# Optimization experiments

Measured on AMD Instinct MI355X. Metric: run time of the kernel, lower is better.

The kernel has to match this reference:

```python
import jax, jax.numpy as jnp
import numpy as np

D_MODEL = 1024
NUM_HEADS = 16
DEPTH = D_MODEL // NUM_HEADS
B, S = 2, 2048


def setup_inputs() -> dict:
    key = jax.random.key(0)
    ks = jax.random.split(key, 13)
    scale = 1.0 / np.sqrt(D_MODEL)
    inp = {
        "v": jax.random.normal(ks[0], (B, S, D_MODEL), jnp.float32),
        "k": jax.random.normal(ks[1], (B, S, D_MODEL), jnp.float32),
        "q": jax.random.normal(ks[2], (B, S, D_MODEL), jnp.float32),
        # additive 0/1 mask, broadcast over heads
        "mask": jax.random.randint(ks[3], (B, 1, S, S), 0, 2).astype(jnp.float32),
        "wq": jax.random.normal(ks[4], (D_MODEL, D_MODEL), jnp.float32) * scale,
        "bq": jnp.zeros((D_MODEL,), jnp.float32),
        "wk": jax.random.normal(ks[5], (D_MODEL, D_MODEL), jnp.float32) * scale,
        "bk": jnp.zeros((D_MODEL,), jnp.float32),
        "wv": jax.random.normal(ks[6], (D_MODEL, D_MODEL), jnp.float32) * scale,
        "bv": jnp.zeros((D_MODEL,), jnp.float32),
        "wo": jax.random.normal(ks[7], (D_MODEL, D_MODEL), jnp.float32) * scale,
        "bo": jnp.zeros((D_MODEL,), jnp.float32),
    }
    return inp


def _split_heads(x):
    # [B, S, D] -> [B, H, S, depth]
    b, s, _ = x.shape
    return x.reshape(b, s, NUM_HEADS, DEPTH).transpose(0, 2, 1, 3)


def reference(v, k, q, mask, wq, bq, wk, bk, wv, bv, wo, bo):
    # torch Linear: y = x @ W.T + b
    qh = _split_heads(q @ wq.T + bq)
    kh = _split_heads(k @ wk.T + bk)
    vh = _split_heads(v @ wv.T + bv)
    score = jnp.einsum("bhqd,bhkd->bhqk", qh, kh) / jnp.sqrt(jnp.float32(DEPTH))
    score = score + mask * jnp.float32(-1e9)
    attn = jax.nn.softmax(score, axis=-1)
    out = jnp.einsum("bhqk,bhkd->bhqd", attn, vh)
    out = out.transpose(0, 2, 1, 3).reshape(out.shape[0], -1, D_MODEL)
    return out @ wo.T + bo
```

## Files before the change

kernel.cpp:

```cpp
#include <hip/hip_runtime.h>


typedef float f32x4 __attribute__((ext_vector_type(4)));
typedef __bf16 bf16x8 __attribute__((ext_vector_type(8)));
typedef unsigned short u16x8 __attribute__((ext_vector_type(8)));

#define DEV static __device__ __forceinline__

DEV unsigned short f2bf(float x) {
  return __builtin_bit_cast(unsigned short, static_cast<__bf16>(x));
}
DEV bf16x8 ld8(const unsigned short* p) {
  return __builtin_bit_cast(bf16x8, *reinterpret_cast<const u16x8*>(p));
}
DEV f32x4 mfma16(bf16x8 a, bf16x8 b, f32x4 c) {
  return __builtin_amdgcn_mfma_f32_16x16x32_bf16(a, b, c, 0, 0, 0);
}
DEV void gl2lds16(const unsigned short* g, unsigned short* l) {
  __builtin_amdgcn_global_load_lds(
      (const __attribute__((address_space(1))) void*)g,
      (__attribute__((address_space(3))) void*)l, 16, 0, 0);
}

__global__ __launch_bounds__(256)
void cvt3(const float* __restrict__ a, const float* __restrict__ b,
          const float* __restrict__ c, unsigned short* __restrict__ oa,
          unsigned short* __restrict__ ob, unsigned short* __restrict__ oc)
{
  const float* in;
  unsigned short* out;
  if (blockIdx.y == 0) { in = a; out = oa; }
  else if (blockIdx.y == 1) { in = b; out = ob; }
  else { in = c; out = oc; }
  const size_t i = (size_t)blockIdx.x * 256 + threadIdx.x;
  const f32x4* p = (const f32x4*)(in + i * 8);
  f32x4 x = p[0], y = p[1];
  u16x8 u;
#pragma unroll
  for (int j = 0; j < 4; ++j) u[j] = f2bf(x[j]);
#pragma unroll
  for (int j = 0; j < 4; ++j) u[4 + j] = f2bf(y[j]);
  *(u16x8*)(out + i * 8) = u;
}

__global__ __launch_bounds__(256)
void cvt4(const float* __restrict__ a, const float* __restrict__ b,
          const float* __restrict__ c, const float* __restrict__ d,
          unsigned short* __restrict__ oa, unsigned short* __restrict__ ob,
          unsigned short* __restrict__ oc, unsigned short* __restrict__ od)
{
  const float* in;
  unsigned short* out;
  if (blockIdx.y == 0) { in = a; out = oa; }
  else if (blockIdx.y == 1) { in = b; out = ob; }
  else if (blockIdx.y == 2) { in = c; out = oc; }
  else { in = d; out = od; }
  const size_t i = (size_t)blockIdx.x * 256 + threadIdx.x;
  const f32x4* p = (const f32x4*)(in + i * 8);
  f32x4 x = p[0], y = p[1];
  u16x8 u;
#pragma unroll
  for (int j = 0; j < 4; ++j) u[j] = f2bf(x[j]);
#pragma unroll
  for (int j = 0; j < 4; ++j) u[4 + j] = f2bf(y[j]);
  *(u16x8*)(out + i * 8) = u;
}

__global__ __launch_bounds__(256)
void mask_bits(const float* __restrict__ m, unsigned long long* __restrict__ bits)
{
  const int l = threadIdx.x & 63;
  int w = blockIdx.x * 4 + (threadIdx.x >> 6);
#pragma unroll 1
  for (int i = 0; i < 16; ++i, w += 8192) {
    float v = m[(size_t)w * 64 + l];
    unsigned long long bl = __ballot(v != 0.0f);
    if (l == 0) bits[w] = bl;
  }
}

template<int MODE>
__global__ __launch_bounds__(256)
void gemm_bf16(const unsigned short* __restrict__ Ab,
               const unsigned short* __restrict__ Wb,
               const float* __restrict__ bias, void* __restrict__ outg,
               float scale)
{
  __shared__ unsigned short lA[128 * 64];
  __shared__ unsigned short lB[64 * 64];
  const int tid = threadIdx.x, lane = tid & 63, wid = tid >> 6;
  const int lr = lane & 15, lg = lane >> 4;
  const int wr = wid >> 1, wc = wid & 1;
  const int mbase = blockIdx.y * 128, nbase = blockIdx.x * 64;
  const int rsub = lane >> 3;
  const int colsw = ((lane & 7) ^ rsub) * 8;

  const f32x4 zf = {0.f, 0.f, 0.f, 0.f};
  f32x4 acc[4][2];
#pragma unroll
  for (int i = 0; i < 4; ++i)
#pragma unroll
    for (int j = 0; j < 2; ++j) acc[i][j] = zf;

  for (int kt = 0; kt < 16; ++kt) {
    const int k0 = kt * 64;
#pragma unroll
    for (int i = 0; i < 4; ++i) {
      const int c = wid + 4 * i;
      const int row = c * 8 + rsub;
      gl2lds16(Ab + (size_t)(mbase + row) * 1024 + k0 + colsw, &lA[c * 512]);
    }
#pragma unroll
    for (int i = 0; i < 2; ++i) {
      const int c = wid + 4 * i;
      const int row = c * 8 + rsub;
      gl2lds16(Wb + (size_t)(nbase + row) * 1024 + k0 + colsw, &lB[c * 512]);
    }
    __syncthreads();

#pragma unroll
    for (int kk = 0; kk < 2; ++kk) {
      const int sw = (((kk * 4 + lg) ^ (lr & 7)) * 8);
      bf16x8 a[4], bb[2];
#pragma unroll
      for (int mi = 0; mi < 4; ++mi)
        a[mi] = ld8(&lA[(wr * 64 + mi * 16 + lr) * 64 + sw]);
#pragma unroll
      for (int ni = 0; ni < 2; ++ni)
        bb[ni] = ld8(&lB[(wc * 32 + ni * 16 + lr) * 64 + sw]);
#pragma unroll
      for (int mi = 0; mi < 4; ++mi)
#pragma unroll
        for (int ni = 0; ni < 2; ++ni)
          acc[mi][ni] = mfma16(a[mi], bb[ni], acc[mi][ni]);
    }
    __syncthreads();
  }

#pragma unroll
  for (int ni = 0; ni < 2; ++ni) {
    const int n = nbase + wc * 32 + ni * 16 + lr;
    const float bv = bias[n];
#pragma unroll
    for (int mi = 0; mi < 4; ++mi) {
#pragma unroll
      for (int r = 0; r < 4; ++r) {
        const int m = mbase + wr * 64 + mi * 16 + lg * 4 + r;
        const float val = (acc[mi][ni][r] + bv) * scale;
        if (MODE == 0) {
          const int b = m >> 11, s = m & 2047, h = n >> 6, d = n & 63;
          ((unsigned short*)outg)[(((size_t)((b * 16 + h) * 2048 + s)) << 6) + d] = f2bf(val);
        } else if (MODE == 1) {
          const int b = m >> 11, s = m & 2047, h = n >> 6, d = n & 63;
          ((unsigned short*)outg)[(((size_t)((b * 16 + h) * 64 + d)) << 11) + s] = f2bf(val);
        } else {
          ((float*)outg)[(size_t)m * 1024 + n] = val;
        }
      }
    }
  }
}

__global__ __launch_bounds__(256)
void attn_fwd(const unsigned short* __restrict__ Qh,
              const unsigned short* __restrict__ Kh,
              const unsigned short* __restrict__ Vt,
              const unsigned long long* __restrict__ bits,
              unsigned short* __restrict__ Ao)
{
  __shared__ unsigned short lK[64][72];
  __shared__ unsigned short lV[64][72];
  __shared__ unsigned short lP[4][16][72];
  const int tid = threadIdx.x, lane = tid & 63, wid = tid >> 6;
  const int lr = lane & 15, lg = lane >> 4;
  const int bh = blockIdx.y;
  const int b = bh >> 4, h = bh & 15;
  const size_t head = (size_t)bh << 17;
  const int qw = blockIdx.x * 64 + wid * 16;

  bf16x8 aq[2];
  {
    const u16x8* qp = (const u16x8*)(Qh + head + ((size_t)(qw + lr) << 6));
    aq[0] = __builtin_bit_cast(bf16x8, qp[lg]);
    aq[1] = __builtin_bit_cast(bf16x8, qp[4 + lg]);
  }

  const f32x4 zf = {0.f, 0.f, 0.f, 0.f};
  f32x4 o[4];
#pragma unroll
  for (int i = 0; i < 4; ++i) o[i] = zf;
  float m_run[4], l_run[4];
#pragma unroll
  for (int r = 0; r < 4; ++r) { m_run[r] = -3.0e38f; l_run[r] = 0.f; }

  const unsigned long long* bptr = bits + ((size_t)b * 2048 + qw) * 32;

  for (int t = 0; t < 32; ++t) {
    const int kv0 = t * 64;
#pragma unroll
    for (int i = 0; i < 2; ++i) {
      int c = tid + 256 * i;
      int row = c >> 3, c8 = c & 7;
      *reinterpret_cast<u16x8*>(&lK[row][c8 * 8]) =
          *(const u16x8*)(Kh + head + ((size_t)(kv0 + row) << 6) + c8 * 8);
      *reinterpret_cast<u16x8*>(&lV[row][c8 * 8]) =
          *(const u16x8*)(Vt + head + ((size_t)row << 11) + kv0 + c8 * 8);
    }
    __syncthreads();

    f32x4 sf[4];
#pragma unroll
    for (int f = 0; f < 4; ++f) {
      f32x4 z = zf;
      z = mfma16(aq[0], ld8(&lK[f * 16 + lr][lg * 8]), z);
      z = mfma16(aq[1], ld8(&lK[f * 16 + lr][32 + lg * 8]), z);
      sf[f] = z;
    }

    float p[4][4];
#pragma unroll
    for (int r = 0; r < 4; ++r) {
      const unsigned long long mb = bptr[(size_t)(lg * 4 + r) * 32 + t];
      float s0 = sf[0][r] - (((mb >> (lr)) & 1) ? 1e9f : 0.f);
      float s1 = sf[1][r] - (((mb >> (16 + lr)) & 1) ? 1e9f : 0.f);
      float s2 = sf[2][r] - (((mb >> (32 + lr)) & 1) ? 1e9f : 0.f);
      float s3 = sf[3][r] - (((mb >> (48 + lr)) & 1) ? 1e9f : 0.f);
      float mx = fmaxf(fmaxf(s0, s1), fmaxf(s2, s3));
      mx = fmaxf(mx, __shfl_xor(mx, 1));
      mx = fmaxf(mx, __shfl_xor(mx, 2));
      mx = fmaxf(mx, __shfl_xor(mx, 4));
      mx = fmaxf(mx, __shfl_xor(mx, 8));
      const float mn = fmaxf(m_run[r], mx);
      const float fac = __expf(m_run[r] - mn);
      m_run[r] = mn;
      float p0 = __expf(s0 - mn), p1 = __expf(s1 - mn);
      float p2 = __expf(s2 - mn), p3 = __expf(s3 - mn);
      p[0][r] = p0; p[1][r] = p1; p[2][r] = p2; p[3][r] = p3;
      float lt = p0 + p1 + p2 + p3;
      lt += __shfl_xor(lt, 1);
      lt += __shfl_xor(lt, 2);
      lt += __shfl_xor(lt, 4);
      lt += __shfl_xor(lt, 8);
      l_run[r] = l_run[r] * fac + lt;
#pragma unroll
      for (int fd = 0; fd < 4; ++fd) o[fd][r] *= fac;
    }

#pragma unroll
    for (int f = 0; f < 4; ++f)
#pragma unroll
      for (int r = 0; r < 4; ++r)
        lP[wid][lg * 4 + r][f * 16 + lr] = f2bf(p[f][r]);

    bf16x8 pa0 = ld8(&lP[wid][lr][lg * 8]);
    bf16x8 pa1 = ld8(&lP[wid][lr][32 + lg * 8]);
#pragma unroll
    for (int fd = 0; fd < 4; ++fd) {
      o[fd] = mfma16(pa0, ld8(&lV[fd * 16 + lr][lg * 8]), o[fd]);
      o[fd] = mfma16(pa1, ld8(&lV[fd * 16 + lr][32 + lg * 8]), o[fd]);
    }
    __syncthreads();
  }

  float inv[4];
#pragma unroll
  for (int r = 0; r < 4; ++r) inv[r] = 1.0f / l_run[r];
  unsigned short* op = Ao + (((size_t)(b * 2048 + blockIdx.x * 64 + wid * 16)) << 10) + h * 64;
#pragma unroll
  for (int fd = 0; fd < 4; ++fd)
#pragma unroll
    for (int r = 0; r < 4; ++r)
      op[((size_t)(lg * 4 + r) << 10) + fd * 16 + lr] = f2bf(o[fd][r] * inv[r]);
}

extern "C" void kernel_launch(void* const* d_in, const int* in_sizes, int n_in,
                              void* d_out, int out_size, void* d_ws, size_t ws_size,
                              hipStream_t stream) {
  const float* v    = (const float*)d_in[0];
  const float* k    = (const float*)d_in[1];
  const float* q    = (const float*)d_in[2];
  const float* mask = (const float*)d_in[3];
  const float* wq = (const float*)d_in[4];  const float* bq = (const float*)d_in[5];
  const float* wk = (const float*)d_in[6];  const float* bk = (const float*)d_in[7];
  const float* wv = (const float*)d_in[8];  const float* bv = (const float*)d_in[9];
  const float* wo = (const float*)d_in[10]; const float* bo = (const float*)d_in[11];

  unsigned short* ws = (unsigned short*)d_ws;
  const size_t T = 4194304;
  unsigned short* Qh  = ws;
  unsigned short* Kh  = ws + T;
  unsigned short* Vt  = ws + 2 * T;
  unsigned short* Ao  = ws + 3 * T;
  unsigned short* Qb  = ws + 4 * T;
  unsigned short* Kb  = ws + 5 * T;
  unsigned short* Vb  = ws + 6 * T;
  unsigned short* Wqb = ws + 7 * T;
  unsigned short* Wkb = Wqb + 1048576;
  unsigned short* Wvb = Wkb + 1048576;
  unsigned short* Wob = Wvb + 1048576;
  unsigned long long* bits = (unsigned long long*)(ws + 8 * T);

  dim3 blk(256);
  cvt3<<<dim3(2048, 3), blk, 0, stream>>>(q, k, v, Qb, Kb, Vb);
  cvt4<<<dim3(512, 4), blk, 0, stream>>>(wq, wk, wv, wo, Wqb, Wkb, Wvb, Wob);
  mask_bits<<<dim3(2048), blk, 0, stream>>>(mask, bits);

  dim3 gg(16, 32);
  gemm_bf16<0><<<gg, blk, 0, stream>>>(Qb, Wqb, bq, Qh, 0.125f);
  gemm_bf16<0><<<gg, blk, 0, stream>>>(Kb, Wkb, bk, Kh, 1.0f);
  gemm_bf16<1><<<gg, blk, 0, stream>>>(Vb, Wvb, bv, Vt, 1.0f);

  attn_fwd<<<dim3(32, 32), blk, 0, stream>>>(Qh, Kh, Vt, bits, Ao);

  gemm_bf16<2><<<gg, blk, 0, stream>>>(Ao, Wob, bo, d_out, 1.0f);
}
```

Before: 341.4 us.

## Transpose attention score layout, swizzle LDS with direct global-to-LDS loads, batch Q/K GEMMs

The attention kernel now computes S^T by swapping the MFMA operands, so each lane holds one query row. Softmax max and sum need only two cross-lane shuffles per tile instead of four per row, and the mask is read once per lane. K and V tiles are loaded straight into XOR-swizzled LDS with global_load_lds instead of going through registers into padded arrays, and P is written with vector stores into a swizzled buffer. The Q and K projection GEMMs are merged into one launch via blockIdx.z, which adds some per-block pointer selection and relies on the swizzle index maths being correct.

```diff
diff --git a/kernel.cpp b/kernel.cpp
--- a/kernel.cpp
+++ b/kernel.cpp
@@ -4,6 +4,7 @@
 typedef float f32x4 __attribute__((ext_vector_type(4)));
 typedef __bf16 bf16x8 __attribute__((ext_vector_type(8)));
 typedef unsigned short u16x8 __attribute__((ext_vector_type(8)));
+typedef unsigned short u16x4 __attribute__((ext_vector_type(4)));
 
 #define DEV static __device__ __forceinline__
 
@@ -81,11 +82,19 @@
 
 template<int MODE>
 __global__ __launch_bounds__(256)
-void gemm_bf16(const unsigned short* __restrict__ Ab,
-               const unsigned short* __restrict__ Wb,
-               const float* __restrict__ bias, void* __restrict__ outg,
-               float scale)
-{
+void gemm_bf16(const unsigned short* __restrict__ A0,
+               const unsigned short* __restrict__ W0,
+               const float* __restrict__ b0, void* __restrict__ o0, float sc0,
+               const unsigned short* __restrict__ A1,
+               const unsigned short* __restrict__ W1,
+               const float* __restrict__ b1, void* __restrict__ o1, float sc1)
+{
+  const unsigned short* Ab = blockIdx.z ? A1 : A0;
+  const unsigned short* Wb = blockIdx.z ? W1 : W0;
+  const float* bias = blockIdx.z ? b1 : b0;
+  void* outg = blockIdx.z ? o1 : o0;
+  const float scale = blockIdx.z ? sc1 : sc0;
+
   __shared__ unsigned short lA[128 * 64];
   __shared__ unsigned short lB[64 * 64];
   const int tid = threadIdx.x, lane = tid & 63, wid = tid >> 6;
@@ -168,11 +177,14 @@
               const unsigned long long* __restrict__ bits,
               unsigned short* __restrict__ Ao)
 {
-  __shared__ unsigned short lK[64][72];
-  __shared__ unsigned short lV[64][72];
-  __shared__ unsigned short lP[4][16][72];
+  __shared__ unsigned short lK[64 * 64];
+  __shared__ unsigned short lV[64 * 64];
+  __shared__ unsigned short lP[4 * 1024];
   const int tid = threadIdx.x, lane = tid & 63, wid = tid >> 6;
   const int lr = lane & 15, lg = lane >> 4;
+  const int a7 = lr & 7;
+  const int rsub = lane >> 3;
+  const int colsw = ((lane & 7) ^ rsub) * 8;
   const int bh = blockIdx.y;
   const int b = bh >> 4, h = bh & 15;
   const size_t head = (size_t)bh << 17;
@@ -189,88 +201,101 @@
   f32x4 o[4];
 #pragma unroll
   for (int i = 0; i < 4; ++i) o[i] = zf;
-  float m_run[4], l_run[4];
-#pragma unroll
-  for (int r = 0; r < 4; ++r) { m_run[r] = -3.0e38f; l_run[r] = 0.f; }
+  float m_run = -3.0e38f, l_run = 0.f;
 
   const unsigned long long* bptr = bits + ((size_t)b * 2048 + qw) * 32;
+  const int g0 = (lg ^ a7) * 8;
+  const int g1 = ((4 + lg) ^ a7) * 8;
 
   for (int t = 0; t < 32; ++t) {
     const int kv0 = t * 64;
 #pragma unroll
     for (int i = 0; i < 2; ++i) {
-      int c = tid + 256 * i;
-      int row = c >> 3, c8 = c & 7;
-      *reinterpret_cast<u16x8*>(&lK[row][c8 * 8]) =
-          *(const u16x8*)(Kh + head + ((size_t)(kv0 + row) << 6) + c8 * 8);
-      *reinterpret_cast<u16x8*>(&lV[row][c8 * 8]) =
-          *(const u16x8*)(Vt + head + ((size_t)row << 11) + kv0 + c8 * 8);
+      const int c = wid + 4 * i;
+      gl2lds16(Kh + head + (size_t)(kv0 + c * 8 + rsub) * 64 + colsw, &lK[c * 512]);
+      gl2lds16(Vt + head + (size_t)(c * 8 + rsub) * 2048 + kv0 + colsw, &lV[c * 512]);
     }
     __syncthreads();
 
     f32x4 sf[4];
 #pragma unroll
     for (int f = 0; f < 4; ++f) {
-      f32x4 z = zf;
-      z = mfma16(aq[0], ld8(&lK[f * 16 + lr][lg * 8]), z);
-      z = mfma16(aq[1], ld8(&lK[f * 16 + lr][32 + lg * 8]), z);
-      sf[f] = z;
-    }
-
-    float p[4][4];
+      const int row = (f * 16 + lr) * 64;
+      f32x4 z = mfma16(ld8(&lK[row + g0]), aq[0], zf);
+      sf[f] = mfma16(ld8(&lK[row + g1]), aq[1], z);
+    }
+
+    const unsigned long long mq = bptr[lr * 32 + t] >> (lg * 4);
+#pragma unroll
+    for (int f = 0; f < 4; ++f) {
+      const unsigned nib = (unsigned)(mq >> (f * 16)) & 0xFu;
+#pragma unroll
+      for (int r = 0; r < 4; ++r)
+        sf[f][r] -= ((nib >> r) & 1u) ? 1e9f : 0.0f;
+    }
+
+    f32x4 mm;
+#pragma unroll
+    for (int r = 0; r < 4; ++r)
+      mm[r] = fmaxf(fmaxf(sf[0][r], sf[1][r]), fmaxf(sf[2][r], sf[3][r]));
+    float mx = fmaxf(fmaxf(mm[0], mm[1]), fmaxf(mm[2], mm[3]));
+    mx = fmaxf(mx, __shfl_xor(mx, 16));
+    mx = fmaxf(mx, __shfl_xor(mx, 32));
+
+    const float mn = fmaxf(m_run, mx);
+    const float fac = __expf(m_run - mn);
+    m_run = mn;
+
+    f32x4 psum = zf;
+    u16x4 pw[4];
+#pragma unroll
+    for (int f = 0; f < 4; ++f) {
+#pragma unroll
+      for (int r = 0; r < 4; ++r) {
+        const float pv = __expf(sf[f][r] - mn);
+        psum[r] += pv;
+        pw[f][r] = f2bf(pv);
+      }
+    }
+    float lt = (psum[0] + psum[1]) + (psum[2] + psum[3]);
+    lt += __shfl_xor(lt, 16);
+    lt += __shfl_xor(lt, 32);
+    l_run = l_run * fac + lt;
+
+#pragma unroll
+    for (int f = 0; f < 4; ++f) {
+      const int g = ((f * 2 + (lg >> 1)) ^ a7) * 8 + (lg & 1) * 4;
+      *(u16x4*)&lP[wid * 1024 + lr * 64 + g] = pw[f];
+    }
+
 #pragma unroll
     for (int r = 0; r < 4; ++r) {
-      const unsigned long long mb = bptr[(size_t)(lg * 4 + r) * 32 + t];
-      float s0 = sf[0][r] - (((mb >> (lr)) & 1) ? 1e9f : 0.f);
-      float s1 = sf[1][r] - (((mb >> (16 + lr)) & 1) ? 1e9f : 0.f);
-      float s2 = sf[2][r] - (((mb >> (32 + lr)) & 1) ? 1e9f : 0.f);
-      float s3 = sf[3][r] - (((mb >> (48 + lr)) & 1) ? 1e9f : 0.f);
-      float mx = fmaxf(fmaxf(s0, s1), fmaxf(s2, s3));
-      mx = fmaxf(mx, __shfl_xor(mx, 1));
-      mx = fmaxf(mx, __shfl_xor(mx, 2));
-      mx = fmaxf(mx, __shfl_xor(mx, 4));
-      mx = fmaxf(mx, __shfl_xor(mx, 8));
-      const float mn = fmaxf(m_run[r], mx);
-      const float fac = __expf(m_run[r] - mn);
-      m_run[r] = mn;
-      float p0 = __expf(s0 - mn), p1 = __expf(s1 - mn);
-      float p2 = __expf(s2 - mn), p3 = __expf(s3 - mn);
-      p[0][r] = p0; p[1][r] = p1; p[2][r] = p2; p[3][r] = p3;
-      float lt = p0 + p1 + p2 + p3;
-      lt += __shfl_xor(lt, 1);
-      lt += __shfl_xor(lt, 2);
-      lt += __shfl_xor(lt, 4);
-      lt += __shfl_xor(lt, 8);
-      l_run[r] = l_run[r] * fac + lt;
-#pragma unroll
-      for (int fd = 0; fd < 4; ++fd) o[fd][r] *= fac;
-    }
-
-#pragma unroll
-    for (int f = 0; f < 4; ++f)
-#pragma unroll
-      for (int r = 0; r < 4; ++r)
-        lP[wid][lg * 4 + r][f * 16 + lr] = f2bf(p[f][r]);
-
-    bf16x8 pa0 = ld8(&lP[wid][lr][lg * 8]);
-    bf16x8 pa1 = ld8(&lP[wid][lr][32 + lg * 8]);
+      const float fr = __shfl(fac, lg * 4 + r);
+#pragma unroll
+      for (int fd = 0; fd < 4; ++fd) o[fd][r] *= fr;
+    }
+
+    bf16x8 pa0 = ld8(&lP[wid * 1024 + lr * 64 + g0]);
+    bf16x8 pa1 = ld8(&lP[wid * 1024 + lr * 64 + g1]);
 #pragma unroll
     for (int fd = 0; fd < 4; ++fd) {
-      o[fd] = mfma16(pa0, ld8(&lV[fd * 16 + lr][lg * 8]), o[fd]);
-      o[fd] = mfma16(pa1, ld8(&lV[fd * 16 + lr][32 + lg * 8]), o[fd]);
+      const int vrow = (fd * 16 + lr) * 64;
+      o[fd] = mfma16(pa0, ld8(&lV[vrow + g0]), o[fd]);
+      o[fd] = mfma16(pa1, ld8(&lV[vrow + g1]), o[fd]);
     }
     __syncthreads();
   }
 
-  float inv[4];
-#pragma unroll
-  for (int r = 0; r < 4; ++r) inv[r] = 1.0f / l_run[r];
+  const float linv = 1.0f / l_run;
+  float invr[4];
+#pragma unroll
+  for (int r = 0; r < 4; ++r) invr[r] = __shfl(linv, lg * 4 + r);
   unsigned short* op = Ao + (((size_t)(b * 2048 + blockIdx.x * 64 + wid * 16)) << 10) + h * 64;
 #pragma unroll
   for (int fd = 0; fd < 4; ++fd)
 #pragma unroll
     for (int r = 0; r < 4; ++r)
-      op[((size_t)(lg * 4 + r) << 10) + fd * 16 + lr] = f2bf(o[fd][r] * inv[r]);
+      op[((size_t)(lg * 4 + r) << 10) + fd * 16 + lr] = f2bf(o[fd][r] * invr[r]);
 }
 
 extern "C" void kernel_launch(void* const* d_in, const int* in_sizes, int n_in,
@@ -305,12 +330,13 @@
   cvt4<<<dim3(512, 4), blk, 0, stream>>>(wq, wk, wv, wo, Wqb, Wkb, Wvb, Wob);
   mask_bits<<<dim3(2048), blk, 0, stream>>>(mask, bits);
 
-  dim3 gg(16, 32);
-  gemm_bf16<0><<<gg, blk, 0, stream>>>(Qb, Wqb, bq, Qh, 0.125f);
-  gemm_bf16<0><<<gg, blk, 0, stream>>>(Kb, Wkb, bk, Kh, 1.0f);
-  gemm_bf16<1><<<gg, blk, 0, stream>>>(Vb, Wvb, bv, Vt, 1.0f);
+  gemm_bf16<0><<<dim3(16, 32, 2), blk, 0, stream>>>(
+      Qb, Wqb, bq, Qh, 0.125f, Kb, Wkb, bk, Kh, 1.0f);
+  gemm_bf16<1><<<dim3(16, 32, 1), blk, 0, stream>>>(
+      Vb, Wvb, bv, Vt, 1.0f, Vb, Wvb, bv, Vt, 1.0f);
 
   attn_fwd<<<dim3(32, 32), blk, 0, stream>>>(Qh, Kh, Vt, bits, Ao);
 
-  gemm_bf16<2><<<gg, blk, 0, stream>>>(Ao, Wob, bo, d_out, 1.0f);
-}
+  gemm_bf16<2><<<dim3(16, 32, 1), blk, 0, stream>>>(
+      Ao, Wob, bo, d_out, 1.0f, Ao, Wob, bo, d_out, 1.0f);
+}
```

After: 302.0 us. 1.13x faster.
